# Kernel optimization log

Measured on AMD Instinct MI355X. Metric: run time of the kernel, lower is better.

Reference implementation:

```python
import jax, jax.numpy as jnp
import numpy as np

H = 8
HD = 128
D = 1024
SCALE = 0.12
EOT = 50256
LN_EPS = 1e-6
THETA = 1024.0


def _layernorm(x, w):
    mu = jnp.mean(x, axis=-1, keepdims=True)
    var = jnp.mean(jnp.square(x - mu), axis=-1, keepdims=True)
    return (x - mu) * jax.lax.rsqrt(var + LN_EPS) * w


def _rmsnorm(x):
    eps = jnp.finfo(x.dtype).eps
    return x * jax.lax.rsqrt(jnp.mean(jnp.square(x), axis=-1, keepdims=True) + eps)


def _rope_tables(seq_len, head_dim):
    # half-truncated RoPE: only first half of the rotation pairs get nonzero freqs
    n = head_dim // 4
    freqs = (1.0 / THETA) ** jnp.linspace(0.0, 1.0, n)
    ang = jnp.concatenate([freqs, jnp.zeros((n,), freqs.dtype)])  # [head_dim//2]
    th = jnp.arange(seq_len, dtype=jnp.float32)[:, None] * ang[None, :]
    return jnp.cos(th), jnp.sin(th)  # each [S, head_dim//2]


def _apply_rope(x, cos, sin):
    # x: [B, S, H, hd]
    x1, x2 = jnp.split(x, 2, axis=-1)
    c = cos[None, :, None, :]
    s = sin[None, :, None, :]
    return jnp.concatenate([x1 * c + x2 * s, -x1 * s + x2 * c], axis=-1)


def setup_inputs() -> dict:
    key = jax.random.key(0)
    ks = jax.random.split(key, 10)
    B, S = 2, 2048
    return {
        "x": jax.random.normal(ks[0], (B, S, D), jnp.float32),
        "value_embed": jax.random.normal(ks[1], (S, D), jnp.float32),
        "x0": jax.random.normal(ks[2], (B, S, D), jnp.float32),
        "lambdas": jax.random.uniform(ks[3], (2,), jnp.float32),
        "sa_lambdas": jax.random.uniform(ks[4], (2,), jnp.float32),
        "ln1_w": jnp.ones((D,), jnp.float32),
        "ln2_w": jnp.ones((D,), jnp.float32),
        "w_qkv": jax.random.normal(ks[5], (D, 3 * D), jnp.float32) * 0.02,
        "w_o": jax.random.normal(ks[6], (D, D), jnp.float32) * 0.02,
        "w_fc": jax.random.normal(ks[7], (D, 4 * D), jnp.float32) * 0.02,
        "w_proj": jax.random.normal(ks[8], (4 * D, D), jnp.float32) * 0.02,
        "input_ids": jax.random.randint(ks[9], (S,), 0, 50257, jnp.int64),
    }


def reference(x, value_embed, x0, lambdas, sa_lambdas, ln1_w, ln2_w,
              w_qkv, w_o, w_fc, w_proj, input_ids):
    B, S, Dm = x.shape
    # U-Net residual mixing
    x = lambdas[0] * x + lambdas[1] * x0

    # attention branch
    xn = _layernorm(x, ln1_w)
    qkv = xn @ w_qkv                                # [B,S,3D]
    q, k, v = jnp.split(qkv, 3, axis=-1)
    q = q.reshape(B, S, H, HD)
    k = k.reshape(B, S, H, HD)
    v = v.reshape(B, S, H, HD)

    cos, sin = _rope_tables(S, HD)
    q = _apply_rope(q, cos, sin)
    k = _apply_rope(k, cos, sin)

    # value-embedding mixing
    ve = value_embed.reshape(S, H, HD)[None]        # [1,S,H,hd]
    v = sa_lambdas[0] * v + sa_lambdas[1] * ve

    # QK norm (unit-weight RMSNorm)
    q = _rmsnorm(q)
    k = _rmsnorm(k)

    # document-aware causal mask
    docs = jnp.cumsum(input_ids == EOT)
    idx = jnp.arange(S)
    mask = (idx[:, None] >= idx[None, :]) & (docs[:, None] == docs[None, :])

    scores = jnp.einsum("bqhd,bkhd->bhqk", q, k) * SCALE
    scores = jnp.where(mask[None, None], scores, -jnp.inf)
    attn = jax.nn.softmax(scores, axis=-1)
    out = jnp.einsum("bhqk,bkhd->bqhd", attn, v).reshape(B, S, Dm)
    x = x + out @ w_o

    # MLP with relu^2
    xn = _layernorm(x, ln2_w)
    h = jnp.square(jax.nn.relu(xn @ w_fc))
    x = x + h @ w_proj
    return x
```

## Files before the change

### kernel.cpp

```cpp
#include <hip/hip_runtime.h>

#define EOT_ID 50256

typedef __attribute__((ext_vector_type(8))) short bf16x8;
typedef __attribute__((ext_vector_type(4))) float f32x4;
typedef __attribute__((ext_vector_type(16))) float f32x16;

#define GLOAD_LDS(g, l)                                                        \
  __builtin_amdgcn_global_load_lds(                                            \
      (const __attribute__((address_space(1))) unsigned int*)(g),              \
      (__attribute__((address_space(3))) unsigned int*)(l), 16, 0, 0)

__device__ __forceinline__ unsigned short f2bf(float f) {
  union { float f; unsigned int u; } v; v.f = f;
  unsigned int r = v.u + 0x7FFFu + ((v.u >> 16) & 1u);
  return (unsigned short)(r >> 16);
}
__device__ __forceinline__ float bf2f(unsigned short b) {
  union { unsigned int u; float f; } v; v.u = ((unsigned int)b) << 16;
  return v.f;
}
__device__ __forceinline__ unsigned int cvtpk(float lo, float hi) {
  unsigned int r;
  asm("v_cvt_pk_bf16_f32 %0, %1, %2" : "=v"(r) : "v"(lo), "v"(hi));
  return r;
}
__device__ __forceinline__ void plswap(unsigned int& a, unsigned int& b) {
  asm volatile("v_permlane32_swap_b32 %0, %1" : "+v"(a), "+v"(b));
}
union U8 { unsigned int u[4]; bf16x8 v; };

__global__ void rope_tab_kernel(float* __restrict__ ct, float* __restrict__ st) {
  const int idx = blockIdx.x * 256 + threadIdx.x;
  const int s = idx >> 5, i = idx & 31;
  const float ang = (float)s * exp2f(-10.0f * (float)i / 31.0f);
  float sv, cv;
  sincosf(ang, &sv, &cv);
  ct[idx] = cv;
  st[idx] = sv;
}

__global__ __launch_bounds__(1024)
void docs_kernel(const int* __restrict__ ids, int* __restrict__ qstart) {
  __shared__ int a[2048], b2[2048];
  const int t = threadIdx.x;
  for (int i = t; i < 2048; i += 1024)
    a[i] = (ids[i] == EOT_ID) ? i : 0;
  __syncthreads();
  int* cur = a; int* nxt = b2;
  for (int off = 1; off < 2048; off <<= 1) {
    for (int i = t; i < 2048; i += 1024) {
      int v = cur[i];
      if (i >= off) { int u = cur[i - off]; v = (u > v) ? u : v; }
      nxt[i] = v;
    }
    __syncthreads();
    int* tmp = cur; cur = nxt; nxt = tmp;
  }
  for (int i = t; i < 2048; i += 1024) qstart[i] = cur[i];
}

__global__ __launch_bounds__(256)
void wtrans_kernel(const float* __restrict__ in, unsigned short* __restrict__ out,
                   int K, int N) {
  __shared__ float tile[32][33];
  const int nb = N >> 5;
  const int k0 = (blockIdx.x / nb) << 5, n0 = (blockIdx.x % nb) << 5;
  const int tx = threadIdx.x & 31, ty = threadIdx.x >> 5;
#pragma unroll
  for (int p = 0; p < 4; p++)
    tile[ty + p * 8][tx] = in[(size_t)(k0 + ty + p * 8) * N + n0 + tx];
  __syncthreads();
#pragma unroll
  for (int p = 0; p < 4; p++)
    out[(size_t)(n0 + ty + p * 8) * K + k0 + tx] = f2bf(tile[tx][ty + p * 8]);
}

__global__ __launch_bounds__(256)
void add5_kernel(const unsigned short* __restrict__ p0,
                 const unsigned short* __restrict__ p1,
                 const unsigned short* __restrict__ p2,
                 const unsigned short* __restrict__ p3,
                 const float* __restrict__ res, float* __restrict__ out) {
  const int i = (blockIdx.x * 256 + threadIdx.x) * 4;
  const ushort4 a = *(const ushort4*)(p0 + i);
  const ushort4 b = *(const ushort4*)(p1 + i);
  const ushort4 c = *(const ushort4*)(p2 + i);
  const ushort4 d = *(const ushort4*)(p3 + i);
  float4 e = *(const float4*)(res + i);
  e.x += bf2f(a.x) + bf2f(b.x) + bf2f(c.x) + bf2f(d.x);
  e.y += bf2f(a.y) + bf2f(b.y) + bf2f(c.y) + bf2f(d.y);
  e.z += bf2f(a.z) + bf2f(b.z) + bf2f(c.z) + bf2f(d.z);
  e.w += bf2f(a.w) + bf2f(b.w) + bf2f(c.w) + bf2f(d.w);
  *(float4*)(out + i) = e;
}

template<bool MIX>
__global__ __launch_bounds__(256)
void ln_kernel(const float* __restrict__ x, const float* __restrict__ x0,
               const float* __restrict__ lam, const float* __restrict__ w,
               float* __restrict__ xm, unsigned short* __restrict__ xn) {
  __shared__ float red[8];
  const int row = blockIdx.x, t = threadIdx.x;
  const size_t base = (size_t)row << 10;
  float4 v = *(const float4*)(x + base + t * 4);
  if (MIX) {
    const float l0 = lam[0], l1 = lam[1];
    const float4 v0 = *(const float4*)(x0 + base + t * 4);
    v.x = l0 * v.x + l1 * v0.x;
    v.y = l0 * v.y + l1 * v0.y;
    v.z = l0 * v.z + l1 * v0.z;
    v.w = l0 * v.w + l1 * v0.w;
    *(float4*)(xm + base + t * 4) = v;
  }
  float s = v.x + v.y + v.z + v.w;
  float q = v.x * v.x + v.y * v.y + v.z * v.z + v.w * v.w;
#pragma unroll
  for (int off = 1; off < 64; off <<= 1) {
    s += __shfl_xor(s, off);
    q += __shfl_xor(q, off);
  }
  const int wid = t >> 6;
  if ((t & 63) == 0) { red[wid] = s; red[4 + wid] = q; }
  __syncthreads();
  s = red[0] + red[1] + red[2] + red[3];
  q = red[4] + red[5] + red[6] + red[7];
  const float mu = s * (1.0f / 1024.0f);
  const float var = q * (1.0f / 1024.0f) - mu * mu;
  const float rstd = rsqrtf(var + 1e-6f);
  const float4 wv = *(const float4*)(w + t * 4);
  ushort4 u;
  u.x = f2bf((v.x - mu) * rstd * wv.x);
  u.y = f2bf((v.y - mu) * rstd * wv.y);
  u.z = f2bf((v.z - mu) * rstd * wv.z);
  u.w = f2bf((v.w - mu) * rstd * wv.w);
  *(ushort4*)(xn + base + t * 4) = u;
}

template<int EPI, int BM, int BK>
__global__ __launch_bounds__(256, 4)
void gemm_bt(const unsigned short* __restrict__ A,
             const unsigned short* __restrict__ Bt,
             void* __restrict__ Cout,
             const float* __restrict__ res,
             int M, int N, int K) {
  __shared__ unsigned short As[2][BM * BK];
  __shared__ unsigned short Bs[2][128 * BK];
  const int t = threadIdx.x;
  const int wid = t >> 6;
  const int lane = t & 63;
  const int ln = lane & 15, kg = lane >> 4;
  const int nbm = M / BM;
  const int xcd = (int)blockIdx.x & 7, rr = (int)blockIdx.x >> 3;
  const int slab = nbm >> 3;
  const int bm = xcd * slab + (rr % slab);
  const int bn = rr / slab;
  const int m0 = bm * BM, n0 = bn << 7;
  const int wrow = (BM == 128) ? ((wid >> 1) * 64) : 0;
  const int wcol = (BM == 128) ? ((wid & 1) * 64) : (wid * 32);
  constexpr int NJ = (BM == 128) ? 4 : 2;
  constexpr int LA = BM * BK / 2048;
  constexpr int LB = 128 * BK / 2048;
  constexpr int KC = BK / 32;

  f32x4 acc[4][NJ] = {};

  const unsigned short* Abase = A + (size_t)m0 * K;
  const unsigned short* Bbase = Bt + (size_t)n0 * K;

  auto swz = [&](int row, int chunk) -> int {
    if constexpr (BK == 32) return chunk ^ ((row >> 1) & 3);
    else                    return chunk ^ (row & 7);
  };

  auto STAGE = [&](int bb, int kt) {
#pragma unroll
    for (int p = 0; p < LA; p++) {
      const int e = t * 8 + p * 2048;
      const int r = e / BK;
      const int cs = swz(r, (e >> 3) & (BK / 8 - 1));
      GLOAD_LDS(Abase + (size_t)r * K + kt + cs * 8, &As[bb][p * 2048 + wid * 512]);
    }
#pragma unroll
    for (int p = 0; p < LB; p++) {
      const int e = t * 8 + p * 2048;
      const int r = e / BK;
      const int cs = swz(r, (e >> 3) & (BK / 8 - 1));
      GLOAD_LDS(Bbase + (size_t)r * K + kt + cs * 8, &Bs[bb][p * 2048 + wid * 512]);
    }
  };

  STAGE(0, 0);
  int cur = 0;
  const int nk = K / BK;
  for (int ki = 0; ki < nk; ki++) {
    if (ki + 1 < nk) {
      STAGE(cur ^ 1, (ki + 1) * BK);
      if constexpr (LA + LB == 4)
        asm volatile("s_waitcnt vmcnt(4)" ::: "memory");
      else
        asm volatile("s_waitcnt vmcnt(6)" ::: "memory");
    } else {
      asm volatile("s_waitcnt vmcnt(0)" ::: "memory");
    }
    __builtin_amdgcn_s_barrier();

#pragma unroll
    for (int c = 0; c < KC; c++) {
      bf16x8 af[4], bfr[NJ];
#pragma unroll
      for (int i = 0; i < 4; i++) {
        const int ra = wrow + i * 16 + ln;
        af[i] = *(const bf16x8*)(&As[cur][ra * BK + swz(ra, c * 4 + kg) * 8]);
      }
#pragma unroll
      for (int j = 0; j < NJ; j++) {
        const int rb = wcol + j * 16 + ln;
        bfr[j] = *(const bf16x8*)(&Bs[cur][rb * BK + swz(rb, c * 4 + kg) * 8]);
      }
#pragma unroll
      for (int i = 0; i < 4; i++)
#pragma unroll
        for (int j = 0; j < NJ; j++)
          acc[i][j] = __builtin_amdgcn_mfma_f32_16x16x32_bf16(af[i], bfr[j], acc[i][j], 0, 0, 0);
    }

    __builtin_amdgcn_s_barrier();
    cur ^= 1;
  }

#pragma unroll
  for (int i = 0; i < 4; i++) {
#pragma unroll
    for (int j = 0; j < NJ; j++) {
#pragma unroll
      for (int r = 0; r < 4; r++) {
        const int row = m0 + wrow + i * 16 + kg * 4 + r;
        const int col = n0 + wcol + j * 16 + ln;
        const size_t idx = (size_t)row * N + col;
        float v = acc[i][j][r];
        if (EPI == 0) {
          ((float*)Cout)[idx] = v;
        } else if (EPI == 1) {
          ((float*)Cout)[idx] = v + res[idx];
        } else if (EPI == 2) {
          v = fmaxf(v, 0.0f);
          ((unsigned short*)Cout)[idx] = f2bf(v * v);
        } else {
          ((unsigned short*)Cout)[idx] = f2bf(v);
        }
      }
    }
  }
}

#define SWZ9(x) ((x) ^ ((((x) >> 9) & 1) << 5))

#define RD_A(BUF, QM)                                                          \
  {                                                                            \
    const char* sb_ = smem + (((BUF)*2 + 0) * 2 + (QM)) * 16384;               \
    _Pragma("unroll") for (int i_ = 0; i_ < 4; i_++)                           \
    _Pragma("unroll") for (int kc_ = 0; kc_ < 2; kc_++) {                      \
      int x_ = kc_ * 8192 + (wr * 64 + i_ * 16 + ln) * 64 + kg * 16;           \
      Af[i_][kc_] = *(const bf16x8*)(sb_ + SWZ9(x_));                          \
    }                                                                          \
  }

#define RD_B(BUF, QN, BARR)                                                    \
  {                                                                            \
    const char* sb_ = smem + (((BUF)*2 + 1) * 2 + (QN)) * 16384;               \
    _Pragma("unroll") for (int j_ = 0; j_ < 2; j_++)                           \
    _Pragma("unroll") for (int kc_ = 0; kc_ < 2; kc_++) {                      \
      int x_ = kc_ * 8192 + (wc * 32 + j_ * 16 + ln) * 64 + kg * 16;           \
      BARR[j_][kc_] = *(const bf16x8*)(sb_ + SWZ9(x_));                        \
    }                                                                          \
  }

#define MFMAQ(QM, QN, BARR)                                                    \
  _Pragma("unroll") for (int i_ = 0; i_ < 4; i_++)                             \
  _Pragma("unroll") for (int j_ = 0; j_ < 2; j_++)                             \
  _Pragma("unroll") for (int kc_ = 0; kc_ < 2; kc_++)                          \
    acc[QM][QN][i_][j_] = __builtin_amdgcn_mfma_f32_16x16x32_bf16(             \
        Af[i_][kc_], BARR[j_][kc_], acc[QM][QN][i_][j_], 0, 0, 0);

#define PHTAIL()                                                               \
  __builtin_amdgcn_s_barrier();                                                \
  asm volatile("s_waitcnt lgkmcnt(0)" ::: "memory");                           \
  __builtin_amdgcn_sched_barrier(0);                                           \
  __builtin_amdgcn_s_setprio(1)

#define PHEND()                                                                \
  __builtin_amdgcn_s_setprio(0);                                               \
  __builtin_amdgcn_s_barrier()

template<int EPI, bool KSPLIT4>
__global__ __launch_bounds__(512, 2)
void gemm256(const unsigned short* __restrict__ A,
             const unsigned short* __restrict__ Bt,
             void* __restrict__ Cout,
             int M, int N, int Kfull, int Klen, int nInner,
             unsigned short* __restrict__ o1, unsigned short* __restrict__ o2,
             unsigned short* __restrict__ o3) {
  extern __shared__ char smem[];
  const int tid = threadIdx.x;
  const int wid = tid >> 6, lane = tid & 63;
  const int wr = wid >> 2, wc = wid & 3;
  const int ln = lane & 15, kg = lane >> 4;
  int blkid = (int)blockIdx.x;
  int split = 0;
  if constexpr (KSPLIT4) {
    split = blkid / nInner;
    blkid -= split * nInner;
  }
  const int nbm = M >> 8;
  const int xcd = blkid & 7, rr = blkid >> 3;
  const int slab = nbm >> 3;
  const int bm = xcd * slab + (rr % slab);
  const int bn = rr / slab;
  const int m0 = bm << 8, n0 = bn << 8;
  const size_t K2 = (size_t)Kfull * 2;
  const size_t kb0 = (size_t)split * Klen * 2;
  const char* Ac = (const char*)A;
  const char* Bc = (const char*)Bt;

  f32x4 acc[2][2][4][2] = {};
  bf16x8 Af[4][2], B0[2][2], B1[2][2];

  auto STG = [&](int buf, int ab, int h, int tile) {
    const char* gb = ab ? Bc : Ac;
    const int ro = (ab ? n0 : m0) + h * 128;
    char* db = smem + ((buf * 2 + ab) * 2 + h) * 16384;
#pragma unroll
    for (int q = 0; q < 2; q++) {
      const int p0 = q * 8192 + tid * 16;
      const int lin = SWZ9(p0);
      GLOAD_LDS(gb + (size_t)(ro + ((lin >> 6) & 127)) * K2 + kb0 +
                    (size_t)tile * 128 + (lin >> 13) * 64 + (lin & 63),
                db + p0);
    }
  };

  STG(0, 0, 0, 0); STG(0, 0, 1, 0); STG(0, 1, 0, 0); STG(0, 1, 1, 0);
  STG(1, 0, 0, 1); STG(1, 1, 0, 1); STG(1, 1, 1, 1);
  asm volatile("s_waitcnt vmcnt(6)" ::: "memory");
  __builtin_amdgcn_s_barrier();

  const int niter = Klen >> 7;
  for (int it = 0; it < niter; it++) {
    const int tA = 2 * it, tB = tA + 1;
    const bool more = (it + 1 < niter);

    RD_A(0, 0); RD_B(0, 0, B0);
    STG(1, 0, 1, tB);
    PHTAIL(); MFMAQ(0, 0, B0); PHEND();
    RD_B(0, 1, B1);
    if (more) STG(0, 0, 0, tA + 2);
    PHTAIL(); MFMAQ(0, 1, B1); PHEND();
    RD_A(0, 1);
    if (more) STG(0, 1, 0, tA + 2);
    PHTAIL(); MFMAQ(1, 0, B0); PHEND();
    if (more) {
      STG(0, 1, 1, tA + 2);
      asm volatile("s_waitcnt vmcnt(6)" ::: "memory");
    } else {
      asm volatile("s_waitcnt vmcnt(0)" ::: "memory");
    }
    PHTAIL(); MFMAQ(1, 1, B1); PHEND();
    RD_A(1, 0); RD_B(1, 0, B0);
    if (more) STG(0, 0, 1, tA + 2);
    PHTAIL(); MFMAQ(0, 0, B0); PHEND();
    RD_B(1, 1, B1);
    if (more) STG(1, 0, 0, tB + 2);
    PHTAIL(); MFMAQ(0, 1, B1); PHEND();
    RD_A(1, 1);
    if (more) STG(1, 1, 0, tB + 2);
    PHTAIL(); MFMAQ(1, 0, B0); PHEND();
    if (more) {
      STG(1, 1, 1, tB + 2);
      asm volatile("s_waitcnt vmcnt(6)" ::: "memory");
    }
    PHTAIL(); MFMAQ(1, 1, B1); PHEND();
  }

  unsigned short* bout = (unsigned short*)Cout;
  if constexpr (KSPLIT4) {
    if (split == 1) bout = o1;
    else if (split == 2) bout = o2;
    else if (split == 3) bout = o3;
  }

#pragma unroll
  for (int qm = 0; qm < 2; qm++)
#pragma unroll
    for (int qn = 0; qn < 2; qn++)
#pragma unroll
      for (int i = 0; i < 4; i++)
#pragma unroll
        for (int j = 0; j < 2; j++)
#pragma unroll
          for (int r = 0; r < 4; r++) {
            const int row = m0 + qm * 128 + wr * 64 + i * 16 + kg * 4 + r;
            const int col = n0 + qn * 128 + wc * 32 + j * 16 + ln;
            const size_t idx = (size_t)row * N + col;
            float v = acc[qm][qn][i][j][r];
            if (EPI == 2) {
              v = fmaxf(v, 0.0f);
              ((unsigned short*)Cout)[idx] = f2bf(v * v);
            } else if (EPI == 3) {
              ((unsigned short*)Cout)[idx] = f2bf(v);
            } else {
              bout[idx] = f2bf(v);
            }
          }
}

__global__ __launch_bounds__(256)
void rope_rms_kernel(const unsigned short* __restrict__ qkv,
                     const float* __restrict__ ct, const float* __restrict__ st,
                     const float* __restrict__ ve, const float* __restrict__ salam,
                     unsigned short* __restrict__ Qh, unsigned short* __restrict__ Kh,
                     unsigned short* __restrict__ Vt) {
  const int t = threadIdx.x;
  const int wid = t >> 6, i = t & 63;
  const int g = blockIdx.x * 4 + wid;
  const int b = g >> 14;
  const int s = (g >> 3) & 2047;
  const int h = g & 7;
  const unsigned short* base = qkv + (size_t)(b * 2048 + s) * 3072 + h * 128;
  float c = 1.0f, sn = 0.0f;
  if (i < 32) { c = ct[s * 32 + i]; sn = st[s * 32 + i]; }
  const float q1 = bf2f(base[i]), q2 = bf2f(base[64 + i]);
  const float k1 = bf2f(base[1024 + i]), k2 = bf2f(base[1024 + 64 + i]);
  const float q1r = q1 * c + q2 * sn, q2r = q2 * c - q1 * sn;
  const float k1r = k1 * c + k2 * sn, k2r = k2 * c - k1 * sn;
  float sq = q1r * q1r + q2r * q2r;
  float sk = k1r * k1r + k2r * k2r;
#pragma unroll
  for (int off = 1; off < 64; off <<= 1) {
    sq += __shfl_xor(sq, off);
    sk += __shfl_xor(sk, off);
  }
  const float eps = 1.1920929e-7f;
  const float rq = rsqrtf(sq * (1.0f / 128.0f) + eps);
  const float rk = rsqrtf(sk * (1.0f / 128.0f) + eps);
  unsigned short* qp = Qh + (((size_t)(b * 2048 + s) * 8 + h) << 7);
  unsigned short* kp = Kh + (((size_t)(b * 2048 + s) * 8 + h) << 7);
  qp[i] = f2bf(q1r * rq); qp[64 + i] = f2bf(q2r * rq);
  kp[i] = f2bf(k1r * rk); kp[64 + i] = f2bf(k2r * rk);
  const float l0 = salam[0], l1 = salam[1];
  const float* vep = ve + (size_t)s * 1024 + h * 128;
  const float v1 = l0 * bf2f(base[2048 + i]) + l1 * vep[i];
  const float v2 = l0 * bf2f(base[2048 + 64 + i]) + l1 * vep[64 + i];
  unsigned short* vp = Vt + (((size_t)(b * 8 + h) * 128) << 11) + s;
  vp[(size_t)i << 11] = f2bf(v1);
  vp[(size_t)(64 + i) << 11] = f2bf(v2);
}

__global__ __launch_bounds__(512, 2)
void attn_kernel(const unsigned short* __restrict__ Qh,
                 const unsigned short* __restrict__ Kh,
                 const unsigned short* __restrict__ Vt,
                 const int* __restrict__ qstart,
                 unsigned short* __restrict__ Out) {
  extern __shared__ char asmem[];

  const int blk = blockIdx.x;
  const int pid = blk >> 4;
  const int bh = blk & 15;
  const int b = bh >> 3, h = bh & 7;
  const int t = threadIdx.x;
  const int wid = t >> 6, lane = t & 63;
  const int qw = wid & 1, kw = wid >> 1;
  const int ln5 = lane & 31, hi = lane >> 5;
  const int tp = qw * 64 + lane;
  const float SC = 0.12f * 1.4426950408889634f;

  unsigned short* Kb = (unsigned short*)(asmem + kw * 16384);
  unsigned short* Vb = (unsigned short*)(asmem + 65536 + kw * 16384);

  auto STAGE = [&](int bb, int kt) {
#pragma unroll
    for (int r = 0; r < 4; r++) {
      const int e = tp * 16 + r * 2048;
      const int row = e >> 8;
      const int ch = (e >> 4) & 15;
      const int sch = ch ^ ((row ^ (row >> 3)) & 7);
      GLOAD_LDS(Kh + (((size_t)(b * 2048 + kt + row) * 8 + h) << 7) + sch * 8,
                (char*)Kb + bb * 8192 + r * 2048 + qw * 1024 + (lane << 4));
    }
#pragma unroll
    for (int r = 0; r < 4; r++) {
      const int e = tp * 16 + r * 2048;
      const int row = e >> 6;
      const int ch = (e >> 4) & 3;
      const int sch = ch ^ ((row >> 1) & 3);
      GLOAD_LDS(Vt + (((size_t)((b * 8 + h) * 128 + row)) << 11) + kt + sch * 8,
                (char*)Vb + bb * 8192 + r * 2048 + qw * 1024 + (lane << 4));
    }
  };

  for (int ph = 0; ph < 2; ph++) {
    const int qt = ph ? (31 - pid) : pid;
    const int q0 = qt << 6;
    const int qrow = q0 + qw * 32;

    bf16x8 qf[8];
    {
      const unsigned short* qp =
          Qh + (((size_t)(b * 2048 + qrow + ln5) * 8 + h) << 7) + hi * 8;
#pragma unroll
      for (int c = 0; c < 8; c++) qf[c] = *(const bf16x8*)(qp + c * 16);
    }
    const int qid = qrow + ln5;
    const int qs = qstart[qid];
    int qsmax = qs;
#pragma unroll
    for (int off = 1; off < 32; off <<= 1)
      qsmax = max(qsmax, __shfl_xor(qsmax, off));

    float m = -64.0f, l = 0.0f;
    f32x16 o[4] = {};

    const int kt0 = qstart[q0] & ~31;
    const int T = (q0 + 64 - kt0) >> 5;

    __syncthreads();
    STAGE(0, kt0 + kw * 32);
    int cur = 0;
    const int nLoop = (T + 3) >> 2;

    for (int i = 0; i < nLoop; i++) {
      const int tid2 = 4 * i + kw;
      const bool hasnext = (tid2 + 4) < T;
      if (hasnext) {
        STAGE(cur ^ 1, kt0 + (tid2 + 4) * 32);
        asm volatile("s_waitcnt vmcnt(8)" ::: "memory");
      } else {
        asm volatile("s_waitcnt vmcnt(0)" ::: "memory");
      }
      __builtin_amdgcn_s_barrier();

      if (tid2 < T) {
        const int kt = kt0 + tid2 * 32;
        const unsigned short* ksb = (const unsigned short*)((char*)Kb + cur * 8192);
        const unsigned short* vsb = (const unsigned short*)((char*)Vb + cur * 8192);

        f32x16 sacc = {};
        {
          const int key = ln5;
          const int kx = (key ^ (key >> 3)) & 7;
          const unsigned short* krow = &ksb[key * 128];
#pragma unroll
          for (int c = 0; c < 8; c++) {
            bf16x8 kf = *(const bf16x8*)(krow + (((2 * c + hi) ^ kx) << 3));
            sacc = __builtin_amdgcn_mfma_f32_32x32x16_bf16(kf, qf[c], sacc, 0, 0, 0);
          }
        }

        const bool full = (kt + 32 <= qrow) && (kt >= qsmax);

        float p[16];
        float mx = -1e30f;
        if (full) {
#pragma unroll
          for (int i2 = 0; i2 < 16; i2++) {
            const float ts = sacc[i2] * SC;
            p[i2] = ts;
            mx = fmaxf(mx, ts);
          }
        } else {
#pragma unroll
          for (int i2 = 0; i2 < 16; i2++) {
            const int key = kt + (i2 & 3) + 8 * (i2 >> 2) + 4 * hi;
            const bool valid = (key <= qid) && (key >= qs);
            const float ts = valid ? sacc[i2] * SC : -1e30f;
            p[i2] = ts;
            mx = fmaxf(mx, ts);
          }
        }
        mx = fmaxf(mx, __shfl_xor(mx, 32));

        const bool dresc = __any(mx - m > 8.0f);
        if (dresc) {
          const float mn = fmaxf(m, mx);
          const float fac = exp2f(m - mn);
          m = mn;
          l *= fac;
#pragma unroll
          for (int r = 0; r < 16; r++) {
            const float fr = __shfl(fac, (r & 3) + 8 * (r >> 2) + 4 * hi);
            o[0][r] *= fr; o[1][r] *= fr; o[2][r] *= fr; o[3][r] *= fr;
          }
        }

        float sum = 0.0f;
#pragma unroll
        for (int i2 = 0; i2 < 16; i2++) {
          const float pv = exp2f(p[i2] - m);
          p[i2] = pv;
          sum += pv;
        }
        sum += __shfl_xor(sum, 32);
        l += sum;

        bf16x8 pa[2];
#pragma unroll
        for (int bb2 = 0; bb2 < 2; bb2++) {
          unsigned int a0 = cvtpk(p[bb2 * 8 + 0], p[bb2 * 8 + 1]);
          unsigned int b0 = cvtpk(p[bb2 * 8 + 4], p[bb2 * 8 + 5]);
          unsigned int a1 = cvtpk(p[bb2 * 8 + 2], p[bb2 * 8 + 3]);
          unsigned int b1 = cvtpk(p[bb2 * 8 + 6], p[bb2 * 8 + 7]);
          plswap(a0, b0);
          plswap(a1, b1);
          U8 u; u.u[0] = a0; u.u[1] = a1; u.u[2] = b0; u.u[3] = b1;
          pa[bb2] = u.v;
        }

#pragma unroll
        for (int dt = 0; dt < 4; dt++) {
          const int d = dt * 32 + ln5;
          const int dx = (d >> 1) & 3;
          const unsigned short* vrow = &vsb[d * 32];
#pragma unroll
          for (int ks = 0; ks < 2; ks++) {
            bf16x8 vf = *(const bf16x8*)(vrow + (((2 * ks + hi) ^ dx) << 3));
            o[dt] = __builtin_amdgcn_mfma_f32_32x32x16_bf16(pa[ks], vf, o[dt], 0, 0, 0);
          }
        }
      }

      __builtin_amdgcn_s_barrier();
      cur ^= 1;
    }

    __syncthreads();
    float* oex = (float*)asmem;
    float* mlx = (float*)(asmem + 99840);
    if (kw != 0) {
      if (lane < 32) {
        mlx[(((kw - 1) * 2 + qw) * 32 + lane) * 2 + 0] = m;
        mlx[(((kw - 1) * 2 + qw) * 32 + lane) * 2 + 1] = l;
      }
      float* dst = oex + (((kw - 1) * 2 + qw) * 64 + lane) * 65;
#pragma unroll
      for (int dt = 0; dt < 4; dt++)
#pragma unroll
        for (int r = 0; r < 16; r++) dst[dt * 16 + r] = o[dt][r];
    }
    __syncthreads();
    if (kw == 0) {
      float mm[3], ll[3];
#pragma unroll
      for (int j = 0; j < 3; j++) {
        mm[j] = mlx[((j * 2 + qw) * 32 + ln5) * 2 + 0];
        ll[j] = mlx[((j * 2 + qw) * 32 + ln5) * 2 + 1];
      }
      const float ms = fmaxf(fmaxf(m, mm[0]), fmaxf(mm[1], mm[2]));
      const float a0 = exp2f(m - ms);
      const float a1 = exp2f(mm[0] - ms);
      const float a2 = exp2f(mm[1] - ms);
      const float a3 = exp2f(mm[2] - ms);
      const float inv = 1.0f / (l * a0 + ll[0] * a1 + ll[1] * a2 + ll[2] * a3);
      const float* s1 = oex + ((0 * 2 + qw) * 64 + lane) * 65;
      const float* s2 = oex + ((1 * 2 + qw) * 64 + lane) * 65;
      const float* s3 = oex + ((2 * 2 + qw) * 64 + lane) * 65;
#pragma unroll
      for (int r = 0; r < 16; r++) {
        const int crow = (r & 3) + 8 * (r >> 2) + 4 * hi;
        const float a0r = __shfl(a0, crow);
        const float a1r = __shfl(a1, crow);
        const float a2r = __shfl(a2, crow);
        const float a3r = __shfl(a3, crow);
        const float ivr = __shfl(inv, crow);
        const int q = qrow + crow;
        unsigned short* op = Out + (((size_t)(b * 2048 + q)) << 10) + h * 128 + ln5;
#pragma unroll
        for (int dt = 0; dt < 4; dt++)
          op[dt * 32] = f2bf((o[dt][r] * a0r + s1[dt * 16 + r] * a1r +
                              s2[dt * 16 + r] * a2r + s3[dt * 16 + r] * a3r) * ivr);
      }
    }
  }
}

extern "C" void kernel_launch(void* const* d_in, const int* in_sizes, int n_in,
                              void* d_out, int out_size, void* d_ws, size_t ws_size,
                              hipStream_t stream) {
  const float* x     = (const float*)d_in[0];
  const float* vemb  = (const float*)d_in[1];
  const float* x0    = (const float*)d_in[2];
  const float* lam   = (const float*)d_in[3];
  const float* slam  = (const float*)d_in[4];
  const float* ln1w  = (const float*)d_in[5];
  const float* ln2w  = (const float*)d_in[6];
  const float* wqkv  = (const float*)d_in[7];
  const float* wo    = (const float*)d_in[8];
  const float* wfc   = (const float*)d_in[9];
  const float* wproj = (const float*)d_in[10];
  const int*   ids   = (const int*)d_in[11];

  char* ws = (char*)d_ws;
  unsigned short* wqkvT  = (unsigned short*)(ws + 0);
  unsigned short* woT    = (unsigned short*)(ws + 6291456);
  unsigned short* wfcT   = (unsigned short*)(ws + 8388608);
  unsigned short* wprojT = (unsigned short*)(ws + 16777216);
  float*          xm     = (float*)(ws + 25165824);
  unsigned short* qkv    = (unsigned short*)(ws + 41943040);
  unsigned short* hbuf   = (unsigned short*)(ws + 41943040);
  unsigned short* xn1    = (unsigned short*)(ws + 92274688);
  unsigned short* ao     = (unsigned short*)(ws + 92274688);
  unsigned short* qh     = (unsigned short*)(ws + 100663296);
  unsigned short* xn2    = (unsigned short*)(ws + 100663296);
  unsigned short* kh     = (unsigned short*)(ws + 109051904);
  unsigned short* vt     = (unsigned short*)(ws + 117440512);
  float*          x2     = (float*)(ws + 109051904);
  float*          ctab   = (float*)(ws + 125829120);
  float*          stab   = (float*)(ws + 126091264);
  int*            qstart = (int*)(ws + 126353408);
  unsigned short* P0 = (unsigned short*)(ws + 0);
  unsigned short* P1 = (unsigned short*)(ws + 8388608);
  unsigned short* P2 = (unsigned short*)(ws + 25165824);
  unsigned short* P3 = (unsigned short*)(ws + 33554432);

  static int attr_done = 0;
  if (!attr_done) {
    hipFuncSetAttribute((const void*)gemm256<3, false>,
                        hipFuncAttributeMaxDynamicSharedMemorySize, 131072);
    hipFuncSetAttribute((const void*)gemm256<2, false>,
                        hipFuncAttributeMaxDynamicSharedMemorySize, 131072);
    hipFuncSetAttribute((const void*)gemm256<4, true>,
                        hipFuncAttributeMaxDynamicSharedMemorySize, 131072);
    hipFuncSetAttribute((const void*)attn_kernel,
                        hipFuncAttributeMaxDynamicSharedMemorySize, 131072);
    attr_done = 1;
  }

  rope_tab_kernel<<<dim3(256), dim3(256), 0, stream>>>(ctab, stab);
  docs_kernel<<<dim3(1), dim3(1024), 0, stream>>>(ids, qstart);
  wtrans_kernel<<<dim3(32 * 96), dim3(256), 0, stream>>>(wqkv, wqkvT, 1024, 3072);
  wtrans_kernel<<<dim3(32 * 32), dim3(256), 0, stream>>>(wo, woT, 1024, 1024);
  wtrans_kernel<<<dim3(32 * 128), dim3(256), 0, stream>>>(wfc, wfcT, 1024, 4096);
  wtrans_kernel<<<dim3(128 * 32), dim3(256), 0, stream>>>(wproj, wprojT, 4096, 1024);

  ln_kernel<true><<<dim3(4096), dim3(256), 0, stream>>>(x, x0, lam, ln1w, xm, xn1);
  gemm256<3, false><<<dim3(192), dim3(512), 131072, stream>>>(
      xn1, wqkvT, (void*)qkv, 4096, 3072, 1024, 1024, 0, nullptr, nullptr, nullptr);
  rope_rms_kernel<<<dim3(8192), dim3(256), 0, stream>>>(qkv, ctab, stab, vemb, slam, qh, kh, vt);
  attn_kernel<<<dim3(256), dim3(512), 131072, stream>>>(qh, kh, vt, qstart, ao);
  gemm_bt<1, 64, 64><<<dim3(64 * 8), dim3(256), 0, stream>>>(ao, woT, (void*)x2, xm,
                                                             4096, 1024, 1024);
  ln_kernel<false><<<dim3(4096), dim3(256), 0, stream>>>(x2, (const float*)nullptr,
                                                         (const float*)nullptr, ln2w,
                                                         (float*)nullptr, xn2);
  gemm256<2, false><<<dim3(256), dim3(512), 131072, stream>>>(
      xn2, wfcT, (void*)hbuf, 4096, 4096, 1024, 1024, 0, nullptr, nullptr, nullptr);
  gemm256<4, true><<<dim3(256), dim3(512), 131072, stream>>>(
      hbuf, wprojT, (void*)P0, 4096, 1024, 4096, 1024, 64, P1, P2, P3);
  add5_kernel<<<dim3(4096), dim3(256), 0, stream>>>(P0, P1, P2, P3, x2, (float*)d_out);
}
```

Baseline: 250.6 us.

## Restructure attention so each wave owns a query tile and streams keys independently

Before, the attention kernel split each 64-query tile's key range across 4 wave groups (split-K) and merged partial softmax state through LDS. Each block also processed two query tiles, pairing short and long causal rows. Now each of 4 waves owns its own 32-query tile. It double-buffers its own K/V tiles in a private 32KB LDS slice with no block barriers and no cross-wave merge. This removes barriers and the reduction epilogue, but the work per wave becomes imbalanced (causal lengths differ) and parallelism per block drops. Grid mapping gives each block 4 consecutive tiles instead of the balanced pairing.

```diff
diff --git a/kernel.cpp b/kernel.cpp
--- a/kernel.cpp
+++ b/kernel.cpp
@@ -456,7 +456,7 @@
   vp[(size_t)(64 + i) << 11] = f2bf(v2);
 }
 
-__global__ __launch_bounds__(512, 2)
+__global__ __launch_bounds__(256, 1)
 void attn_kernel(const unsigned short* __restrict__ Qh,
                  const unsigned short* __restrict__ Kh,
                  const unsigned short* __restrict__ Vt,
@@ -465,221 +465,169 @@
   extern __shared__ char asmem[];
 
   const int blk = blockIdx.x;
-  const int pid = blk >> 4;
+  const int grp = blk >> 4;
   const int bh = blk & 15;
   const int b = bh >> 3, h = bh & 7;
   const int t = threadIdx.x;
   const int wid = t >> 6, lane = t & 63;
-  const int qw = wid & 1, kw = wid >> 1;
+  const int jt = grp * 4 + wid;
+  const int qrow = jt * 32;
   const int ln5 = lane & 31, hi = lane >> 5;
-  const int tp = qw * 64 + lane;
   const float SC = 0.12f * 1.4426950408889634f;
 
-  unsigned short* Kb = (unsigned short*)(asmem + kw * 16384);
-  unsigned short* Vb = (unsigned short*)(asmem + 65536 + kw * 16384);
+  char* wbase = asmem + wid * 32768;
 
   auto STAGE = [&](int bb, int kt) {
 #pragma unroll
-    for (int r = 0; r < 4; r++) {
-      const int e = tp * 16 + r * 2048;
+    for (int r = 0; r < 8; r++) {
+      const int e = lane * 16 + r * 1024;
       const int row = e >> 8;
       const int ch = (e >> 4) & 15;
       const int sch = ch ^ ((row ^ (row >> 3)) & 7);
       GLOAD_LDS(Kh + (((size_t)(b * 2048 + kt + row) * 8 + h) << 7) + sch * 8,
-                (char*)Kb + bb * 8192 + r * 2048 + qw * 1024 + (lane << 4));
-    }
-#pragma unroll
-    for (int r = 0; r < 4; r++) {
-      const int e = tp * 16 + r * 2048;
+                wbase + bb * 16384 + r * 1024 + (lane << 4));
+    }
+#pragma unroll
+    for (int r = 0; r < 8; r++) {
+      const int e = lane * 16 + r * 1024;
       const int row = e >> 6;
       const int ch = (e >> 4) & 3;
       const int sch = ch ^ ((row >> 1) & 3);
       GLOAD_LDS(Vt + (((size_t)((b * 8 + h) * 128 + row)) << 11) + kt + sch * 8,
-                (char*)Vb + bb * 8192 + r * 2048 + qw * 1024 + (lane << 4));
+                wbase + bb * 16384 + 8192 + r * 1024 + (lane << 4));
     }
   };
 
-  for (int ph = 0; ph < 2; ph++) {
-    const int qt = ph ? (31 - pid) : pid;
-    const int q0 = qt << 6;
-    const int qrow = q0 + qw * 32;
-
-    bf16x8 qf[8];
+  bf16x8 qf[8];
+  {
+    const unsigned short* qp =
+        Qh + (((size_t)(b * 2048 + qrow + ln5) * 8 + h) << 7) + hi * 8;
+#pragma unroll
+    for (int c = 0; c < 8; c++) qf[c] = *(const bf16x8*)(qp + c * 16);
+  }
+  const int qid = qrow + ln5;
+  const int qs = qstart[qid];
+  int qsmax = qs;
+#pragma unroll
+  for (int off = 1; off < 32; off <<= 1)
+    qsmax = max(qsmax, __shfl_xor(qsmax, off));
+
+  float m = -64.0f, l = 0.0f;
+  f32x16 o[4] = {};
+
+  const int kt0 = qstart[qrow] & ~31;
+  const int kend = qrow + 32;
+
+  STAGE(0, kt0);
+  int cur = 0;
+
+  for (int kt = kt0; kt < kend; kt += 32) {
+    if (kt + 32 < kend) {
+      STAGE(cur ^ 1, kt + 32);
+      asm volatile("s_waitcnt vmcnt(16)" ::: "memory");
+    } else {
+      asm volatile("s_waitcnt vmcnt(0)" ::: "memory");
+    }
+
+    const unsigned short* ksb = (const unsigned short*)(wbase + cur * 16384);
+    const unsigned short* vsb = (const unsigned short*)(wbase + cur * 16384 + 8192);
+
+    f32x16 sacc = {};
     {
-      const unsigned short* qp =
-          Qh + (((size_t)(b * 2048 + qrow + ln5) * 8 + h) << 7) + hi * 8;
-#pragma unroll
-      for (int c = 0; c < 8; c++) qf[c] = *(const bf16x8*)(qp + c * 16);
-    }
-    const int qid = qrow + ln5;
-    const int qs = qstart[qid];
-    int qsmax = qs;
-#pragma unroll
-    for (int off = 1; off < 32; off <<= 1)
-      qsmax = max(qsmax, __shfl_xor(qsmax, off));
-
-    float m = -64.0f, l = 0.0f;
-    f32x16 o[4] = {};
-
-    const int kt0 = qstart[q0] & ~31;
-    const int T = (q0 + 64 - kt0) >> 5;
-
-    __syncthreads();
-    STAGE(0, kt0 + kw * 32);
-    int cur = 0;
-    const int nLoop = (T + 3) >> 2;
-
-    for (int i = 0; i < nLoop; i++) {
-      const int tid2 = 4 * i + kw;
-      const bool hasnext = (tid2 + 4) < T;
-      if (hasnext) {
-        STAGE(cur ^ 1, kt0 + (tid2 + 4) * 32);
-        asm volatile("s_waitcnt vmcnt(8)" ::: "memory");
-      } else {
-        asm volatile("s_waitcnt vmcnt(0)" ::: "memory");
+      const int key = ln5;
+      const int kx = (key ^ (key >> 3)) & 7;
+      const unsigned short* krow = &ksb[key * 128];
+#pragma unroll
+      for (int c = 0; c < 8; c++) {
+        bf16x8 kf = *(const bf16x8*)(krow + (((2 * c + hi) ^ kx) << 3));
+        sacc = __builtin_amdgcn_mfma_f32_32x32x16_bf16(kf, qf[c], sacc, 0, 0, 0);
       }
-      __builtin_amdgcn_s_barrier();
-
-      if (tid2 < T) {
-        const int kt = kt0 + tid2 * 32;
-        const unsigned short* ksb = (const unsigned short*)((char*)Kb + cur * 8192);
-        const unsigned short* vsb = (const unsigned short*)((char*)Vb + cur * 8192);
-
-        f32x16 sacc = {};
-        {
-          const int key = ln5;
-          const int kx = (key ^ (key >> 3)) & 7;
-          const unsigned short* krow = &ksb[key * 128];
-#pragma unroll
-          for (int c = 0; c < 8; c++) {
-            bf16x8 kf = *(const bf16x8*)(krow + (((2 * c + hi) ^ kx) << 3));
-            sacc = __builtin_amdgcn_mfma_f32_32x32x16_bf16(kf, qf[c], sacc, 0, 0, 0);
-          }
-        }
-
-        const bool full = (kt + 32 <= qrow) && (kt >= qsmax);
-
-        float p[16];
-        float mx = -1e30f;
-        if (full) {
-#pragma unroll
-          for (int i2 = 0; i2 < 16; i2++) {
-            const float ts = sacc[i2] * SC;
-            p[i2] = ts;
-            mx = fmaxf(mx, ts);
-          }
-        } else {
-#pragma unroll
-          for (int i2 = 0; i2 < 16; i2++) {
-            const int key = kt + (i2 & 3) + 8 * (i2 >> 2) + 4 * hi;
-            const bool valid = (key <= qid) && (key >= qs);
-            const float ts = valid ? sacc[i2] * SC : -1e30f;
-            p[i2] = ts;
-            mx = fmaxf(mx, ts);
-          }
-        }
-        mx = fmaxf(mx, __shfl_xor(mx, 32));
-
-        const bool dresc = __any(mx - m > 8.0f);
-        if (dresc) {
-          const float mn = fmaxf(m, mx);
-          const float fac = exp2f(m - mn);
-          m = mn;
-          l *= fac;
-#pragma unroll
-          for (int r = 0; r < 16; r++) {
-            const float fr = __shfl(fac, (r & 3) + 8 * (r >> 2) + 4 * hi);
-            o[0][r] *= fr; o[1][r] *= fr; o[2][r] *= fr; o[3][r] *= fr;
-          }
-        }
-
-        float sum = 0.0f;
-#pragma unroll
-        for (int i2 = 0; i2 < 16; i2++) {
-          const float pv = exp2f(p[i2] - m);
-          p[i2] = pv;
-          sum += pv;
-        }
-        sum += __shfl_xor(sum, 32);
-        l += sum;
-
-        bf16x8 pa[2];
-#pragma unroll
-        for (int bb2 = 0; bb2 < 2; bb2++) {
-          unsigned int a0 = cvtpk(p[bb2 * 8 + 0], p[bb2 * 8 + 1]);
-          unsigned int b0 = cvtpk(p[bb2 * 8 + 4], p[bb2 * 8 + 5]);
-          unsigned int a1 = cvtpk(p[bb2 * 8 + 2], p[bb2 * 8 + 3]);
-          unsigned int b1 = cvtpk(p[bb2 * 8 + 6], p[bb2 * 8 + 7]);
-          plswap(a0, b0);
-          plswap(a1, b1);
-          U8 u; u.u[0] = a0; u.u[1] = a1; u.u[2] = b0; u.u[3] = b1;
-          pa[bb2] = u.v;
-        }
-
-#pragma unroll
-        for (int dt = 0; dt < 4; dt++) {
-          const int d = dt * 32 + ln5;
-          const int dx = (d >> 1) & 3;
-          const unsigned short* vrow = &vsb[d * 32];
-#pragma unroll
-          for (int ks = 0; ks < 2; ks++) {
-            bf16x8 vf = *(const bf16x8*)(vrow + (((2 * ks + hi) ^ dx) << 3));
-            o[dt] = __builtin_amdgcn_mfma_f32_32x32x16_bf16(pa[ks], vf, o[dt], 0, 0, 0);
-          }
-        }
+    }
+
+    const bool full = (kt + 32 <= qrow) && (kt >= qsmax);
+
+    float p[16];
+    float mx = -1e30f;
+    if (full) {
+#pragma unroll
+      for (int i2 = 0; i2 < 16; i2++) {
+        const float ts = sacc[i2] * SC;
+        p[i2] = ts;
+        mx = fmaxf(mx, ts);
       }
-
-      __builtin_amdgcn_s_barrier();
-      cur ^= 1;
-    }
-
-    __syncthreads();
-    float* oex = (float*)asmem;
-    float* mlx = (float*)(asmem + 99840);
-    if (kw != 0) {
-      if (lane < 32) {
-        mlx[(((kw - 1) * 2 + qw) * 32 + lane) * 2 + 0] = m;
-        mlx[(((kw - 1) * 2 + qw) * 32 + lane) * 2 + 1] = l;
+    } else {
+#pragma unroll
+      for (int i2 = 0; i2 < 16; i2++) {
+        const int key = kt + (i2 & 3) + 8 * (i2 >> 2) + 4 * hi;
+        const bool valid = (key <= qid) && (key >= qs);
+        const float ts = valid ? sacc[i2] * SC : -1e30f;
+        p[i2] = ts;
+        mx = fmaxf(mx, ts);
       }
-      float* dst = oex + (((kw - 1) * 2 + qw) * 64 + lane) * 65;
-#pragma unroll
-      for (int dt = 0; dt < 4; dt++)
-#pragma unroll
-        for (int r = 0; r < 16; r++) dst[dt * 16 + r] = o[dt][r];
-    }
-    __syncthreads();
-    if (kw == 0) {
-      float mm[3], ll[3];
-#pragma unroll
-      for (int j = 0; j < 3; j++) {
-        mm[j] = mlx[((j * 2 + qw) * 32 + ln5) * 2 + 0];
-        ll[j] = mlx[((j * 2 + qw) * 32 + ln5) * 2 + 1];
+    }
+    mx = fmaxf(mx, __shfl_xor(mx, 32));
+
+    const bool dresc = __any(mx - m > 8.0f);
+    if (dresc) {
+      const float mn = fmaxf(m, mx);
+      const float fac = exp2f(m - mn);
+      m = mn;
+      l *= fac;
+#pragma unroll
+      for (int r = 0; r < 16; r++) {
+        const float fr = __shfl(fac, (r & 3) + 8 * (r >> 2) + 4 * hi);
+        o[0][r] *= fr; o[1][r] *= fr; o[2][r] *= fr; o[3][r] *= fr;
       }
-      const float ms = fmaxf(fmaxf(m, mm[0]), fmaxf(mm[1], mm[2]));
-      const float a0 = exp2f(m - ms);
-      const float a1 = exp2f(mm[0] - ms);
-      const float a2 = exp2f(mm[1] - ms);
-      const float a3 = exp2f(mm[2] - ms);
-      const float inv = 1.0f / (l * a0 + ll[0] * a1 + ll[1] * a2 + ll[2] * a3);
-      const float* s1 = oex + ((0 * 2 + qw) * 64 + lane) * 65;
-      const float* s2 = oex + ((1 * 2 + qw) * 64 + lane) * 65;
-      const float* s3 = oex + ((2 * 2 + qw) * 64 + lane) * 65;
-#pragma unroll
-      for (int r = 0; r < 16; r++) {
-        const int crow = (r & 3) + 8 * (r >> 2) + 4 * hi;
-        const float a0r = __shfl(a0, crow);
-        const float a1r = __shfl(a1, crow);
-        const float a2r = __shfl(a2, crow);
-        const float a3r = __shfl(a3, crow);
-        const float ivr = __shfl(inv, crow);
-        const int q = qrow + crow;
-        unsigned short* op = Out + (((size_t)(b * 2048 + q)) << 10) + h * 128 + ln5;
-#pragma unroll
-        for (int dt = 0; dt < 4; dt++)
-          op[dt * 32] = f2bf((o[dt][r] * a0r + s1[dt * 16 + r] * a1r +
-                              s2[dt * 16 + r] * a2r + s3[dt * 16 + r] * a3r) * ivr);
+    }
+
+    float sum = 0.0f;
+#pragma unroll
+    for (int i2 = 0; i2 < 16; i2++) {
+      const float pv = exp2f(p[i2] - m);
+      p[i2] = pv;
+      sum += pv;
+    }
+    sum += __shfl_xor(sum, 32);
+    l += sum;
+
+    bf16x8 pa[2];
+#pragma unroll
+    for (int bb2 = 0; bb2 < 2; bb2++) {
+      unsigned int a0 = cvtpk(p[bb2 * 8 + 0], p[bb2 * 8 + 1]);
+      unsigned int b0 = cvtpk(p[bb2 * 8 + 4], p[bb2 * 8 + 5]);
+      unsigned int a1 = cvtpk(p[bb2 * 8 + 2], p[bb2 * 8 + 3]);
+      unsigned int b1 = cvtpk(p[bb2 * 8 + 6], p[bb2 * 8 + 7]);
+      plswap(a0, b0);
+      plswap(a1, b1);
+      U8 u; u.u[0] = a0; u.u[1] = a1; u.u[2] = b0; u.u[3] = b1;
+      pa[bb2] = u.v;
+    }
+
+#pragma unroll
+    for (int dt = 0; dt < 4; dt++) {
+      const int d = dt * 32 + ln5;
+      const int dx = (d >> 1) & 3;
+      const unsigned short* vrow = &vsb[d * 32];
+#pragma unroll
+      for (int ks = 0; ks < 2; ks++) {
+        bf16x8 vf = *(const bf16x8*)(vrow + (((2 * ks + hi) ^ dx) << 3));
+        o[dt] = __builtin_amdgcn_mfma_f32_32x32x16_bf16(pa[ks], vf, o[dt], 0, 0, 0);
       }
     }
+
+    cur ^= 1;
+  }
+
+  const float inv = 1.0f / l;
+#pragma unroll
+  for (int r = 0; r < 16; r++) {
+    const int crow = (r & 3) + 8 * (r >> 2) + 4 * hi;
+    const float ivr = __shfl(inv, crow);
+    const int q = qrow + crow;
+    unsigned short* op = Out + (((size_t)(b * 2048 + q)) << 10) + h * 128 + ln5;
+#pragma unroll
+    for (int dt = 0; dt < 4; dt++)
+      op[dt * 32] = f2bf(o[dt][r] * ivr);
   }
 }
 
@@ -746,7 +694,7 @@
   gemm256<3, false><<<dim3(192), dim3(512), 131072, stream>>>(
       xn1, wqkvT, (void*)qkv, 4096, 3072, 1024, 1024, 0, nullptr, nullptr, nullptr);
   rope_rms_kernel<<<dim3(8192), dim3(256), 0, stream>>>(qkv, ctab, stab, vemb, slam, qh, kh, vt);
-  attn_kernel<<<dim3(256), dim3(512), 131072, stream>>>(qh, kh, vt, qstart, ao);
+  attn_kernel<<<dim3(256), dim3(256), 131072, stream>>>(qh, kh, vt, qstart, ao);
   gemm_bt<1, 64, 64><<<dim3(64 * 8), dim3(256), 0, stream>>>(ao, woT, (void*)x2, xm,
                                                              4096, 1024, 1024);
   ln_kernel<false><<<dim3(4096), dim3(256), 0, stream>>>(x2, (const float*)nullptr,
```

New measurement: 301.8 us. 20.4% more time.

## Split attention blocks into per-32-query halves with private per-wave KV tiles

Applied to the files above, without the earlier changes.

The attention kernel now launches twice as many 256-thread blocks, each handling a 32-row query half with four waves that split the key tiles among themselves. Each wave stages its own K/V tile into a private LDS region and waits on it, so the shared double-buffered staging and block-wide barriers in the key loop are gone. This is meant to cut barrier stalls, start each half at its own document boundary to skip masked tiles, and raise occupancy through smaller LDS use. The cost is no prefetch overlap: every wave waits for its loads to finish before computing, and K/V data is no longer shared between the two query halves.

```diff
diff --git a/kernel.cpp b/kernel.cpp
--- a/kernel.cpp
+++ b/kernel.cpp
@@ -456,7 +456,7 @@
   vp[(size_t)(64 + i) << 11] = f2bf(v2);
 }
 
-__global__ __launch_bounds__(512, 2)
+__global__ __launch_bounds__(256, 2)
 void attn_kernel(const unsigned short* __restrict__ Qh,
                  const unsigned short* __restrict__ Kh,
                  const unsigned short* __restrict__ Vt,
@@ -465,44 +465,44 @@
   extern __shared__ char asmem[];
 
   const int blk = blockIdx.x;
-  const int pid = blk >> 4;
+  const int pid = blk >> 5;
+  const int qhalf = (blk >> 4) & 1;
   const int bh = blk & 15;
   const int b = bh >> 3, h = bh & 7;
   const int t = threadIdx.x;
   const int wid = t >> 6, lane = t & 63;
-  const int qw = wid & 1, kw = wid >> 1;
   const int ln5 = lane & 31, hi = lane >> 5;
-  const int tp = qw * 64 + lane;
   const float SC = 0.12f * 1.4426950408889634f;
 
-  unsigned short* Kb = (unsigned short*)(asmem + kw * 16384);
-  unsigned short* Vb = (unsigned short*)(asmem + 65536 + kw * 16384);
-
-  auto STAGE = [&](int bb, int kt) {
-#pragma unroll
-    for (int r = 0; r < 4; r++) {
-      const int e = tp * 16 + r * 2048;
+  char* Kb = asmem + wid * 16384;
+  char* Vb = Kb + 8192;
+
+  auto STAGE = [&](int kt) {
+#pragma unroll
+    for (int r = 0; r < 8; r++) {
+      const int e = lane * 16 + r * 1024;
       const int row = e >> 8;
       const int ch = (e >> 4) & 15;
       const int sch = ch ^ ((row ^ (row >> 3)) & 7);
       GLOAD_LDS(Kh + (((size_t)(b * 2048 + kt + row) * 8 + h) << 7) + sch * 8,
-                (char*)Kb + bb * 8192 + r * 2048 + qw * 1024 + (lane << 4));
-    }
-#pragma unroll
-    for (int r = 0; r < 4; r++) {
-      const int e = tp * 16 + r * 2048;
+                Kb + r * 1024 + (lane << 4));
+    }
+#pragma unroll
+    for (int r = 0; r < 8; r++) {
+      const int e = lane * 16 + r * 1024;
       const int row = e >> 6;
       const int ch = (e >> 4) & 3;
       const int sch = ch ^ ((row >> 1) & 3);
       GLOAD_LDS(Vt + (((size_t)((b * 8 + h) * 128 + row)) << 11) + kt + sch * 8,
-                (char*)Vb + bb * 8192 + r * 2048 + qw * 1024 + (lane << 4));
+                Vb + r * 1024 + (lane << 4));
     }
   };
 
   for (int ph = 0; ph < 2; ph++) {
     const int qt = ph ? (31 - pid) : pid;
+    const int qh2 = ph ? (qhalf ^ 1) : qhalf;
     const int q0 = qt << 6;
-    const int qrow = q0 + qw * 32;
+    const int qrow = q0 + qh2 * 32;
 
     bf16x8 qf[8];
     {
@@ -521,139 +521,124 @@
     float m = -64.0f, l = 0.0f;
     f32x16 o[4] = {};
 
-    const int kt0 = qstart[q0] & ~31;
-    const int T = (q0 + 64 - kt0) >> 5;
+    const int kt0 = qstart[qrow] & ~31;
+    const int T = (qrow + 32 - kt0) >> 5;
 
     __syncthreads();
-    STAGE(0, kt0 + kw * 32);
-    int cur = 0;
-    const int nLoop = (T + 3) >> 2;
-
-    for (int i = 0; i < nLoop; i++) {
-      const int tid2 = 4 * i + kw;
-      const bool hasnext = (tid2 + 4) < T;
-      if (hasnext) {
-        STAGE(cur ^ 1, kt0 + (tid2 + 4) * 32);
-        asm volatile("s_waitcnt vmcnt(8)" ::: "memory");
+
+    for (int tid2 = wid; tid2 < T; tid2 += 4) {
+      const int kt = kt0 + tid2 * 32;
+      STAGE(kt);
+      asm volatile("s_waitcnt vmcnt(0)" ::: "memory");
+
+      const unsigned short* ksb = (const unsigned short*)Kb;
+      const unsigned short* vsb = (const unsigned short*)Vb;
+
+      f32x16 sacc = {};
+      {
+        const int key = ln5;
+        const int kx = (key ^ (key >> 3)) & 7;
+        const unsigned short* krow = &ksb[key * 128];
+#pragma unroll
+        for (int c = 0; c < 8; c++) {
+          bf16x8 kf = *(const bf16x8*)(krow + (((2 * c + hi) ^ kx) << 3));
+          sacc = __builtin_amdgcn_mfma_f32_32x32x16_bf16(kf, qf[c], sacc, 0, 0, 0);
+        }
+      }
+
+      const bool full = (kt + 32 <= qrow) && (kt >= qsmax);
+
+      float p[16];
+      float mx = -1e30f;
+      if (full) {
+#pragma unroll
+        for (int i2 = 0; i2 < 16; i2++) {
+          const float ts = sacc[i2] * SC;
+          p[i2] = ts;
+          mx = fmaxf(mx, ts);
+        }
       } else {
-        asm volatile("s_waitcnt vmcnt(0)" ::: "memory");
-      }
-      __builtin_amdgcn_s_barrier();
-
-      if (tid2 < T) {
-        const int kt = kt0 + tid2 * 32;
-        const unsigned short* ksb = (const unsigned short*)((char*)Kb + cur * 8192);
-        const unsigned short* vsb = (const unsigned short*)((char*)Vb + cur * 8192);
-
-        f32x16 sacc = {};
-        {
-          const int key = ln5;
-          const int kx = (key ^ (key >> 3)) & 7;
-          const unsigned short* krow = &ksb[key * 128];
-#pragma unroll
-          for (int c = 0; c < 8; c++) {
-            bf16x8 kf = *(const bf16x8*)(krow + (((2 * c + hi) ^ kx) << 3));
-            sacc = __builtin_amdgcn_mfma_f32_32x32x16_bf16(kf, qf[c], sacc, 0, 0, 0);
-          }
+#pragma unroll
+        for (int i2 = 0; i2 < 16; i2++) {
+          const int key = kt + (i2 & 3) + 8 * (i2 >> 2) + 4 * hi;
+          const bool valid = (key <= qid) && (key >= qs);
+          const float ts = valid ? sacc[i2] * SC : -1e30f;
+          p[i2] = ts;
+          mx = fmaxf(mx, ts);
         }
-
-        const bool full = (kt + 32 <= qrow) && (kt >= qsmax);
-
-        float p[16];
-        float mx = -1e30f;
-        if (full) {
-#pragma unroll
-          for (int i2 = 0; i2 < 16; i2++) {
-            const float ts = sacc[i2] * SC;
-            p[i2] = ts;
-            mx = fmaxf(mx, ts);
-          }
-        } else {
-#pragma unroll
-          for (int i2 = 0; i2 < 16; i2++) {
-            const int key = kt + (i2 & 3) + 8 * (i2 >> 2) + 4 * hi;
-            const bool valid = (key <= qid) && (key >= qs);
-            const float ts = valid ? sacc[i2] * SC : -1e30f;
-            p[i2] = ts;
-            mx = fmaxf(mx, ts);
-          }
+      }
+      mx = fmaxf(mx, __shfl_xor(mx, 32));
+
+      const bool dresc = __any(mx - m > 8.0f);
+      if (dresc) {
+        const float mn = fmaxf(m, mx);
+        const float fac = exp2f(m - mn);
+        m = mn;
+        l *= fac;
+#pragma unroll
+        for (int r = 0; r < 16; r++) {
+          const float fr = __shfl(fac, (r & 3) + 8 * (r >> 2) + 4 * hi);
+          o[0][r] *= fr; o[1][r] *= fr; o[2][r] *= fr; o[3][r] *= fr;
         }
-        mx = fmaxf(mx, __shfl_xor(mx, 32));
-
-        const bool dresc = __any(mx - m > 8.0f);
-        if (dresc) {
-          const float mn = fmaxf(m, mx);
-          const float fac = exp2f(m - mn);
-          m = mn;
-          l *= fac;
-#pragma unroll
-          for (int r = 0; r < 16; r++) {
-            const float fr = __shfl(fac, (r & 3) + 8 * (r >> 2) + 4 * hi);
-            o[0][r] *= fr; o[1][r] *= fr; o[2][r] *= fr; o[3][r] *= fr;
-          }
+      }
+
+      float sum = 0.0f;
+#pragma unroll
+      for (int i2 = 0; i2 < 16; i2++) {
+        const float pv = exp2f(p[i2] - m);
+        p[i2] = pv;
+        sum += pv;
+      }
+      sum += __shfl_xor(sum, 32);
+      l += sum;
+
+      bf16x8 pa[2];
+#pragma unroll
+      for (int bb2 = 0; bb2 < 2; bb2++) {
+        unsigned int a0 = cvtpk(p[bb2 * 8 + 0], p[bb2 * 8 + 1]);
+        unsigned int b0 = cvtpk(p[bb2 * 8 + 4], p[bb2 * 8 + 5]);
+        unsigned int a1 = cvtpk(p[bb2 * 8 + 2], p[bb2 * 8 + 3]);
+        unsigned int b1 = cvtpk(p[bb2 * 8 + 6], p[bb2 * 8 + 7]);
+        plswap(a0, b0);
+        plswap(a1, b1);
+        U8 u; u.u[0] = a0; u.u[1] = a1; u.u[2] = b0; u.u[3] = b1;
+        pa[bb2] = u.v;
+      }
+
+#pragma unroll
+      for (int dt = 0; dt < 4; dt++) {
+        const int d = dt * 32 + ln5;
+        const int dx = (d >> 1) & 3;
+        const unsigned short* vrow = &vsb[d * 32];
+#pragma unroll
+        for (int ks = 0; ks < 2; ks++) {
+          bf16x8 vf = *(const bf16x8*)(vrow + (((2 * ks + hi) ^ dx) << 3));
+          o[dt] = __builtin_amdgcn_mfma_f32_32x32x16_bf16(pa[ks], vf, o[dt], 0, 0, 0);
         }
-
-        float sum = 0.0f;
-#pragma unroll
-        for (int i2 = 0; i2 < 16; i2++) {
-          const float pv = exp2f(p[i2] - m);
-          p[i2] = pv;
-          sum += pv;
-        }
-        sum += __shfl_xor(sum, 32);
-        l += sum;
-
-        bf16x8 pa[2];
-#pragma unroll
-        for (int bb2 = 0; bb2 < 2; bb2++) {
-          unsigned int a0 = cvtpk(p[bb2 * 8 + 0], p[bb2 * 8 + 1]);
-          unsigned int b0 = cvtpk(p[bb2 * 8 + 4], p[bb2 * 8 + 5]);
-          unsigned int a1 = cvtpk(p[bb2 * 8 + 2], p[bb2 * 8 + 3]);
-          unsigned int b1 = cvtpk(p[bb2 * 8 + 6], p[bb2 * 8 + 7]);
-          plswap(a0, b0);
-          plswap(a1, b1);
-          U8 u; u.u[0] = a0; u.u[1] = a1; u.u[2] = b0; u.u[3] = b1;
-          pa[bb2] = u.v;
-        }
-
-#pragma unroll
-        for (int dt = 0; dt < 4; dt++) {
-          const int d = dt * 32 + ln5;
-          const int dx = (d >> 1) & 3;
-          const unsigned short* vrow = &vsb[d * 32];
-#pragma unroll
-          for (int ks = 0; ks < 2; ks++) {
-            bf16x8 vf = *(const bf16x8*)(vrow + (((2 * ks + hi) ^ dx) << 3));
-            o[dt] = __builtin_amdgcn_mfma_f32_32x32x16_bf16(pa[ks], vf, o[dt], 0, 0, 0);
-          }
-        }
-      }
-
-      __builtin_amdgcn_s_barrier();
-      cur ^= 1;
+      }
     }
 
     __syncthreads();
     float* oex = (float*)asmem;
-    float* mlx = (float*)(asmem + 99840);
-    if (kw != 0) {
+    float* mlx = (float*)(asmem + 49920);
+    if (wid != 0) {
       if (lane < 32) {
-        mlx[(((kw - 1) * 2 + qw) * 32 + lane) * 2 + 0] = m;
-        mlx[(((kw - 1) * 2 + qw) * 32 + lane) * 2 + 1] = l;
-      }
-      float* dst = oex + (((kw - 1) * 2 + qw) * 64 + lane) * 65;
+        mlx[((wid - 1) * 32 + lane) * 2 + 0] = m;
+        mlx[((wid - 1) * 32 + lane) * 2 + 1] = l;
+      }
+      float* dst = oex + ((wid - 1) * 64 + lane) * 65;
 #pragma unroll
       for (int dt = 0; dt < 4; dt++)
 #pragma unroll
         for (int r = 0; r < 16; r++) dst[dt * 16 + r] = o[dt][r];
     }
     __syncthreads();
-    if (kw == 0) {
+    if (wid == 0) {
       float mm[3], ll[3];
 #pragma unroll
       for (int j = 0; j < 3; j++) {
-        mm[j] = mlx[((j * 2 + qw) * 32 + ln5) * 2 + 0];
-        ll[j] = mlx[((j * 2 + qw) * 32 + ln5) * 2 + 1];
+        mm[j] = mlx[(j * 32 + ln5) * 2 + 0];
+        ll[j] = mlx[(j * 32 + ln5) * 2 + 1];
       }
       const float ms = fmaxf(fmaxf(m, mm[0]), fmaxf(mm[1], mm[2]));
       const float a0 = exp2f(m - ms);
@@ -661,9 +646,9 @@
       const float a2 = exp2f(mm[1] - ms);
       const float a3 = exp2f(mm[2] - ms);
       const float inv = 1.0f / (l * a0 + ll[0] * a1 + ll[1] * a2 + ll[2] * a3);
-      const float* s1 = oex + ((0 * 2 + qw) * 64 + lane) * 65;
-      const float* s2 = oex + ((1 * 2 + qw) * 64 + lane) * 65;
-      const float* s3 = oex + ((2 * 2 + qw) * 64 + lane) * 65;
+      const float* s1 = oex + (0 * 64 + lane) * 65;
+      const float* s2 = oex + (1 * 64 + lane) * 65;
+      const float* s3 = oex + (2 * 64 + lane) * 65;
 #pragma unroll
       for (int r = 0; r < 16; r++) {
         const int crow = (r & 3) + 8 * (r >> 2) + 4 * hi;
@@ -731,7 +716,7 @@
     hipFuncSetAttribute((const void*)gemm256<4, true>,
                         hipFuncAttributeMaxDynamicSharedMemorySize, 131072);
     hipFuncSetAttribute((const void*)attn_kernel,
-                        hipFuncAttributeMaxDynamicSharedMemorySize, 131072);
+                        hipFuncAttributeMaxDynamicSharedMemorySize, 65536);
     attr_done = 1;
   }
 
@@ -746,7 +731,7 @@
   gemm256<3, false><<<dim3(192), dim3(512), 131072, stream>>>(
       xn1, wqkvT, (void*)qkv, 4096, 3072, 1024, 1024, 0, nullptr, nullptr, nullptr);
   rope_rms_kernel<<<dim3(8192), dim3(256), 0, stream>>>(qkv, ctab, stab, vemb, slam, qh, kh, vt);
-  attn_kernel<<<dim3(256), dim3(512), 131072, stream>>>(qh, kh, vt, qstart, ao);
+  attn_kernel<<<dim3(512), dim3(256), 65536, stream>>>(qh, kh, vt, qstart, ao);
   gemm_bt<1, 64, 64><<<dim3(64 * 8), dim3(256), 0, stream>>>(ao, woT, (void*)x2, xm,
                                                              4096, 1024, 1024);
   ln_kernel<false><<<dim3(4096), dim3(256), 0, stream>>>(x2, (const float*)nullptr,
```

After: 253.7 us. Within noise of the previous version (+1.2%).
